# Optimization experiments

Measured on AMD Instinct MI355X. Metric: run time of the kernel, lower is better.

## Reference

```python
import jax, jax.numpy as jnp
import numpy as np

N_NODES = 40000
N_EDGES = 640000
D = 128
NEG_SLOPE = 0.2
EPS = 0.0  # init_eps=0, learn_eps=False -> constant buffer


def setup_inputs() -> dict:
    key = jax.random.key(0)
    ks = jax.random.split(key, 9)
    return {
        "feat": jax.random.normal(ks[0], (N_NODES, D), dtype=jnp.float32),
        "W_src": jax.random.normal(ks[1], (D, D), dtype=jnp.float32) * 0.1,
        "W_dst": jax.random.normal(ks[2], (D, D), dtype=jnp.float32) * 0.1,
        "W_src2": jax.random.normal(ks[3], (D, D), dtype=jnp.float32) * 0.1,
        "W_dst2": jax.random.normal(ks[4], (D, D), dtype=jnp.float32) * 0.1,
        "attn_l": jax.random.normal(ks[5], (D,), dtype=jnp.float32) * 0.1,
        "attn_r": jax.random.normal(ks[6], (D,), dtype=jnp.float32) * 0.1,
        "src": jax.random.randint(ks[7], (N_EDGES,), 0, N_NODES, dtype=jnp.int32),
        "dst": jax.random.randint(ks[8], (N_EDGES,), 0, N_NODES, dtype=jnp.int32),
    }


def reference(feat, W_src, W_dst, W_src2, W_dst2, attn_l, attn_r, src, dst):
    n = feat.shape[0]
    # Four linear projections (no bias), nn.Linear applies x @ W.T
    fs1 = feat @ W_src.T    # [N, D] -> messages for GIN sum
    fd1 = feat @ W_dst.T    # [N, D] -> self term
    fs2 = feat @ W_src2.T   # [N, D] -> attention-weighted messages
    fd2 = feat @ W_dst2.T   # [N, D]

    # GAT-style per-node attention logits
    el = jnp.sum(fs2 * attn_l, axis=-1)  # [N]
    er = jnp.sum(fd2 * attn_r, axis=-1)  # [N]

    # Per-edge score: u_add_v + leaky_relu
    e = el[src] + er[dst]                                   # [E]
    e = jnp.where(e >= 0, e, NEG_SLOPE * e)

    # edge_softmax: segment-wise softmax over edges grouped by dst
    seg_max = jax.ops.segment_max(e, dst, num_segments=n)   # [N]
    seg_max = jnp.where(jnp.isfinite(seg_max), seg_max, 0.0)
    ex = jnp.exp(e - seg_max[dst])                          # [E]
    denom = jax.ops.segment_sum(ex, dst, num_segments=n)    # [N]
    a = ex / denom[dst]                                     # [E]

    # update_all(copy_u, sum): plain neighbor sum of fs1
    neigh = jax.ops.segment_sum(fs1[src], dst, num_segments=n)            # [N, D]
    # update_all(u_mul_e, sum): attention-weighted sum of fs2
    add_ft = jax.ops.segment_sum(fs2[src] * a[:, None], dst, num_segments=n)  # [N, D]

    rst = (1.0 + EPS) * fd1 + neigh + add_ft
    return rst
```

## Files before the change

kernel.cpp:

```cpp
#include <hip/hip_runtime.h>
#include <math.h>

#define N_NODES 40000
#define N_EDGES 640000
#define D 128
#define NEG_SLOPE 0.2f
#define BCAP 64

typedef __bf16 bf16x8 __attribute__((ext_vector_type(8)));
typedef float f32x4 __attribute__((ext_vector_type(4)));

__device__ __forceinline__ unsigned short f2bf(float f) {
    unsigned int u = __float_as_uint(f);
    return (unsigned short)((u + 0x7fffu + ((u >> 16) & 1u)) >> 16);
}
__device__ __forceinline__ float bflo(unsigned int u) { return __uint_as_float(u << 16); }
__device__ __forceinline__ float bfhi(unsigned int u) { return __uint_as_float(u & 0xffff0000u); }

__global__ void k_zero(uint4* __restrict__ cnt4) {
    int i = blockIdx.x * 256 + threadIdx.x;
    if (i < 10000) cnt4[i] = make_uint4(0, 0, 0, 0);
}

__global__ void k_init_fill(const float* __restrict__ Ws, const float* __restrict__ Ws2,
                            const float* __restrict__ Wd, const float* __restrict__ Wd2,
                            const float* __restrict__ attn_l, const float* __restrict__ attn_r,
                            unsigned short* __restrict__ Wfrag,
                            float* __restrict__ v_l, float* __restrict__ v_r,
                            const int* __restrict__ src, const int* __restrict__ dst,
                            int* __restrict__ cnt, unsigned short* __restrict__ bucket,
                            const float* __restrict__ feat, unsigned int* __restrict__ featb) {
    if (blockIdx.x >= 2693) {
        int t = (blockIdx.x - 2693) * 256 + threadIdx.x;
        if (t < 640000) {
            const float* fp = feat + (size_t)t * 8;
            float4 p = *(const float4*)fp;
            float4 q = *(const float4*)(fp + 4);
            uint4 u;
            u.x = (unsigned int)f2bf(p.x) | ((unsigned int)f2bf(p.y) << 16);
            u.y = (unsigned int)f2bf(p.z) | ((unsigned int)f2bf(p.w) << 16);
            u.z = (unsigned int)f2bf(q.x) | ((unsigned int)f2bf(q.y) << 16);
            u.w = (unsigned int)f2bf(q.z) | ((unsigned int)f2bf(q.w) << 16);
            *(uint4*)(featb + (size_t)t * 4) = u;
        }
        return;
    }
    if (blockIdx.x >= 193) {
        int e = (blockIdx.x - 193) * 256 + threadIdx.x;
        if (e < N_EDGES) {
            int d = dst[e];
            int slot = atomicAdd(&cnt[d], 1);
            if (slot < BCAP) bucket[(size_t)d * BCAP + slot] = (unsigned short)src[e];
        }
        return;
    }
    if (blockIdx.x == 192) {
        int t = threadIdx.x;
        if (t < 128) {
            float s = 0.0f;
            for (int j = 0; j < D; ++j) s += attn_l[j] * Ws2[j * D + t];
            v_l[t] = s;
        } else {
            int k = t - 128;
            float s = 0.0f;
            for (int j = 0; j < D; ++j) s += attn_r[j] * Wd2[j * D + k];
            v_r[k] = s;
        }
        return;
    }
    int idx = blockIdx.x * 256 + threadIdx.x;
    int e    = idx & 7;
    int lane = (idx >> 3) & 63;
    int ks   = (idx >> 9) & 3;
    int ct   = (idx >> 11) & 7;
    int m    = idx >> 14;
    int col  = ct * 16 + (lane & 15);
    int k    = ks * 32 + (lane >> 4) * 8 + e;
    const float* W = (m == 0) ? Ws : (m == 1) ? Ws2 : Wd;
    Wfrag[idx] = f2bf(W[col * D + k]);
}

__global__ __launch_bounds__(256) void k_gemm_pre(
    const float* __restrict__ feat, const unsigned short* __restrict__ Wfrag,
    const float* __restrict__ vl, const float* __restrict__ vr,
    float* __restrict__ out, float* __restrict__ el, float* __restrict__ er)
{
    const int lane = threadIdx.x & 63;
    const int wave = threadIdx.x >> 6;
    const int row0 = blockIdx.x * 64 + wave * 16;
    const int arow = row0 + (lane & 15);
    const int kb   = (lane >> 4) * 8;

    bf16x8 a[4];
    float sl = 0.f, sr = 0.f;
    #pragma unroll
    for (int ks = 0; ks < 4; ++ks) {
        const float* fp = feat + (size_t)arow * D + ks * 32 + kb;
        float4 p = *(const float4*)fp;
        float4 q = *(const float4*)(fp + 4);
        bf16x8 av;
        av[0] = (__bf16)p.x; av[1] = (__bf16)p.y; av[2] = (__bf16)p.z; av[3] = (__bf16)p.w;
        av[4] = (__bf16)q.x; av[5] = (__bf16)q.y; av[6] = (__bf16)q.z; av[7] = (__bf16)q.w;
        a[ks] = av;
        const float* vlp = vl + ks * 32 + kb;
        const float* vrp = vr + ks * 32 + kb;
        float4 l0 = *(const float4*)vlp, l1 = *(const float4*)(vlp + 4);
        float4 r0 = *(const float4*)vrp, r1 = *(const float4*)(vrp + 4);
        sl += p.x*l0.x + p.y*l0.y + p.z*l0.z + p.w*l0.w
            + q.x*l1.x + q.y*l1.y + q.z*l1.z + q.w*l1.w;
        sr += p.x*r0.x + p.y*r0.y + p.z*r0.z + p.w*r0.w
            + q.x*r1.x + q.y*r1.y + q.z*r1.z + q.w*r1.w;
    }
    sl += __shfl_xor(sl, 16); sl += __shfl_xor(sl, 32);
    sr += __shfl_xor(sr, 16); sr += __shfl_xor(sr, 32);
    if (lane < 16) { el[row0 + lane] = sl; er[row0 + lane] = sr; }

    const bf16x8* wf = (const bf16x8*)Wfrag + (size_t)(2 * 8 * 4) * 64;
    f32x4 acc[8];
    #pragma unroll
    for (int ct = 0; ct < 8; ++ct) acc[ct] = (f32x4){0.f, 0.f, 0.f, 0.f};
    #pragma unroll
    for (int ks = 0; ks < 4; ++ks) {
        #pragma unroll
        for (int ct = 0; ct < 8; ++ct) {
            bf16x8 b = wf[(size_t)(ct * 4 + ks) * 64 + lane];
            acc[ct] = __builtin_amdgcn_mfma_f32_16x16x32_bf16(a[ks], b, acc[ct], 0, 0, 0);
        }
    }

    const int rbase = row0 + (lane >> 4) * 4;
    const int cbase = lane & 15;
    #pragma unroll
    for (int ct = 0; ct < 8; ++ct)
        #pragma unroll
        for (int r = 0; r < 4; ++r)
            out[(size_t)(rbase + r) * D + ct * 16 + cbase] = acc[ct][r];
}

__global__ __launch_bounds__(256) void k_aggregate(
    const int* __restrict__ cnt, const unsigned short* __restrict__ bucket,
    const float* __restrict__ el, const float* __restrict__ er,
    const unsigned int* __restrict__ featb,
    unsigned int* __restrict__ agg1b, unsigned int* __restrict__ agg2b)
{
    const int node = blockIdx.x * 4 + (threadIdx.x >> 6);
    const int lane = threadIdx.x & 63;
    if (node >= N_NODES) return;
    int deg = cnt[node];
    deg = (deg > BCAP) ? BCAP : deg;

    const int q = lane & 15;
    const int g = lane >> 4;
    float A1[8], A2[8];
    #pragma unroll
    for (int c = 0; c < 8; ++c) { A1[c] = 0.f; A2[c] = 0.f; }

    if (deg > 0) {
        const int base = node * BCAP;
        const float ern = er[node];
        int s_l = 0;
        float e = -INFINITY;
        if (lane < deg) {
            s_l = bucket[base + lane];
            e = el[s_l] + ern;
            e = (e >= 0.f) ? e : NEG_SLOPE * e;
        }
        float mx = e;
        #pragma unroll
        for (int w = 32; w >= 1; w >>= 1) mx = fmaxf(mx, __shfl_xor(mx, w));
        float p = (lane < deg) ? __expf(e - mx) : 0.f;
        float ssum = p;
        #pragma unroll
        for (int w = 32; w >= 1; w >>= 1) ssum += __shfl_xor(ssum, w);
        float a_l = p / ssum;

        const int dup = (deg + 15) & ~15;
        for (int i = 0; i < dup; i += 16) {
            uint4 v[4];
            float av[4], wf[4];
            #pragma unroll
            for (int j = 0; j < 4; ++j) {
                int eidx = i + j * 4 + g;
                int s = __shfl(s_l, eidx);
                av[j] = __shfl(a_l, eidx);
                wf[j] = (eidx < deg) ? 1.0f : 0.0f;
                v[j] = *(const uint4*)(featb + (size_t)s * 64 + q * 4);
            }
            #pragma unroll
            for (int j = 0; j < 4; ++j) {
                float x0 = bflo(v[j].x), x1 = bfhi(v[j].x);
                float x2 = bflo(v[j].y), x3 = bfhi(v[j].y);
                float x4 = bflo(v[j].z), x5 = bfhi(v[j].z);
                float x6 = bflo(v[j].w), x7 = bfhi(v[j].w);
                A1[0] += wf[j] * x0; A2[0] += av[j] * x0;
                A1[1] += wf[j] * x1; A2[1] += av[j] * x1;
                A1[2] += wf[j] * x2; A2[2] += av[j] * x2;
                A1[3] += wf[j] * x3; A2[3] += av[j] * x3;
                A1[4] += wf[j] * x4; A2[4] += av[j] * x4;
                A1[5] += wf[j] * x5; A2[5] += av[j] * x5;
                A1[6] += wf[j] * x6; A2[6] += av[j] * x6;
                A1[7] += wf[j] * x7; A2[7] += av[j] * x7;
            }
        }
        #pragma unroll
        for (int c = 0; c < 8; ++c) {
            A1[c] += __shfl_xor(A1[c], 16); A1[c] += __shfl_xor(A1[c], 32);
            A2[c] += __shfl_xor(A2[c], 16); A2[c] += __shfl_xor(A2[c], 32);
        }
    }

    if (lane < 16) {
        uint4 u1, u2;
        u1.x = (unsigned int)f2bf(A1[0]) | ((unsigned int)f2bf(A1[1]) << 16);
        u1.y = (unsigned int)f2bf(A1[2]) | ((unsigned int)f2bf(A1[3]) << 16);
        u1.z = (unsigned int)f2bf(A1[4]) | ((unsigned int)f2bf(A1[5]) << 16);
        u1.w = (unsigned int)f2bf(A1[6]) | ((unsigned int)f2bf(A1[7]) << 16);
        u2.x = (unsigned int)f2bf(A2[0]) | ((unsigned int)f2bf(A2[1]) << 16);
        u2.y = (unsigned int)f2bf(A2[2]) | ((unsigned int)f2bf(A2[3]) << 16);
        u2.z = (unsigned int)f2bf(A2[4]) | ((unsigned int)f2bf(A2[5]) << 16);
        u2.w = (unsigned int)f2bf(A2[6]) | ((unsigned int)f2bf(A2[7]) << 16);
        *(uint4*)(agg1b + (size_t)node * 64 + q * 4) = u1;
        *(uint4*)(agg2b + (size_t)node * 64 + q * 4) = u2;
    }
}

__global__ __launch_bounds__(256) void k_gemm_post(
    const unsigned int* __restrict__ agg1b, const unsigned int* __restrict__ agg2b,
    const unsigned short* __restrict__ Wfrag, float* __restrict__ out)
{
    const int lane = threadIdx.x & 63;
    const int wave = threadIdx.x >> 6;
    const int row0 = blockIdx.x * 64 + wave * 16;
    const int arow = row0 + (lane & 15);
    const int kb   = (lane >> 4) * 8;

    bf16x8 a1[4], a2[4];
    #pragma unroll
    for (int ks = 0; ks < 4; ++ks) {
        a1[ks] = *(const bf16x8*)((const unsigned short*)agg1b + (size_t)arow * D + ks * 32 + kb);
        a2[ks] = *(const bf16x8*)((const unsigned short*)agg2b + (size_t)arow * D + ks * 32 + kb);
    }

    const bf16x8* wf0 = (const bf16x8*)Wfrag;
    const bf16x8* wf1 = (const bf16x8*)Wfrag + (size_t)(8 * 4) * 64;
    f32x4 acc[8];
    #pragma unroll
    for (int ct = 0; ct < 8; ++ct) acc[ct] = (f32x4){0.f, 0.f, 0.f, 0.f};
    #pragma unroll
    for (int ks = 0; ks < 4; ++ks) {
        #pragma unroll
        for (int ct = 0; ct < 8; ++ct) {
            acc[ct] = __builtin_amdgcn_mfma_f32_16x16x32_bf16(a1[ks], wf0[(size_t)(ct * 4 + ks) * 64 + lane], acc[ct], 0, 0, 0);
            acc[ct] = __builtin_amdgcn_mfma_f32_16x16x32_bf16(a2[ks], wf1[(size_t)(ct * 4 + ks) * 64 + lane], acc[ct], 0, 0, 0);
        }
    }

    const int rbase = row0 + (lane >> 4) * 4;
    const int cbase = lane & 15;
    #pragma unroll
    for (int ct = 0; ct < 8; ++ct)
        #pragma unroll
        for (int r = 0; r < 4; ++r) {
            size_t o = (size_t)(rbase + r) * D + ct * 16 + cbase;
            out[o] += acc[ct][r];
        }
}

extern "C" void kernel_launch(void* const* d_in, const int* in_sizes, int n_in,
                              void* d_out, int out_size, void* d_ws, size_t ws_size,
                              hipStream_t stream) {
    const float* feat   = (const float*)d_in[0];
    const float* W_src  = (const float*)d_in[1];
    const float* W_dst  = (const float*)d_in[2];
    const float* W_src2 = (const float*)d_in[3];
    const float* W_dst2 = (const float*)d_in[4];
    const float* attn_l = (const float*)d_in[5];
    const float* attn_r = (const float*)d_in[6];
    const int*   src    = (const int*)d_in[7];
    const int*   dst    = (const int*)d_in[8];
    float* out = (float*)d_out;

    char* w = (char*)d_ws;
    float* v_l = (float*)w;                       w += 128 * 4;
    float* v_r = (float*)w;                       w += 128 * 4;
    float* el  = (float*)w;                       w += N_NODES * 4;
    float* er  = (float*)w;                       w += N_NODES * 4;
    int* cnt   = (int*)w;                         w += N_NODES * 4;
    unsigned int* featb = (unsigned int*)w;       w += (size_t)N_NODES * 64 * 4;
    unsigned int* agg1b = (unsigned int*)w;       w += (size_t)N_NODES * 64 * 4;
    unsigned int* agg2b = (unsigned int*)w;       w += (size_t)N_NODES * 64 * 4;
    unsigned short* bucket = (unsigned short*)w;  w += (size_t)N_NODES * BCAP * 2;
    unsigned short* Wfrag = (unsigned short*)w;   w += 3 * 8 * 4 * 64 * 8 * 2;

    k_zero<<<40, 256, 0, stream>>>((uint4*)cnt);

    k_init_fill<<<5193, 256, 0, stream>>>(
        W_src, W_src2, W_dst, W_dst2, attn_l, attn_r, Wfrag, v_l, v_r,
        src, dst, cnt, bucket, feat, featb);

    k_gemm_pre<<<625, 256, 0, stream>>>(feat, Wfrag, v_l, v_r, out, el, er);

    k_aggregate<<<(N_NODES + 3) / 4, 256, 0, stream>>>(cnt, bucket, el, er,
                                                       featb, agg1b, agg2b);

    k_gemm_post<<<625, 256, 0, stream>>>(agg1b, agg2b, Wfrag, out);
}
```

Baseline: 102.2 us.

## Fuse self-term GEMM into post-aggregation GEMM and compute logits during bf16 conversion

Result: faster. 96.21 us (-5.8%).

```diff
diff --git a/kernel.cpp b/kernel.cpp
--- a/kernel.cpp
+++ b/kernel.cpp
@@ -17,44 +17,11 @@
 __device__ __forceinline__ float bflo(unsigned int u) { return __uint_as_float(u << 16); }
 __device__ __forceinline__ float bfhi(unsigned int u) { return __uint_as_float(u & 0xffff0000u); }
 
-__global__ void k_zero(uint4* __restrict__ cnt4) {
-    int i = blockIdx.x * 256 + threadIdx.x;
-    if (i < 10000) cnt4[i] = make_uint4(0, 0, 0, 0);
-}
-
-__global__ void k_init_fill(const float* __restrict__ Ws, const float* __restrict__ Ws2,
-                            const float* __restrict__ Wd, const float* __restrict__ Wd2,
-                            const float* __restrict__ attn_l, const float* __restrict__ attn_r,
-                            unsigned short* __restrict__ Wfrag,
-                            float* __restrict__ v_l, float* __restrict__ v_r,
-                            const int* __restrict__ src, const int* __restrict__ dst,
-                            int* __restrict__ cnt, unsigned short* __restrict__ bucket,
-                            const float* __restrict__ feat, unsigned int* __restrict__ featb) {
-    if (blockIdx.x >= 2693) {
-        int t = (blockIdx.x - 2693) * 256 + threadIdx.x;
-        if (t < 640000) {
-            const float* fp = feat + (size_t)t * 8;
-            float4 p = *(const float4*)fp;
-            float4 q = *(const float4*)(fp + 4);
-            uint4 u;
-            u.x = (unsigned int)f2bf(p.x) | ((unsigned int)f2bf(p.y) << 16);
-            u.y = (unsigned int)f2bf(p.z) | ((unsigned int)f2bf(p.w) << 16);
-            u.z = (unsigned int)f2bf(q.x) | ((unsigned int)f2bf(q.y) << 16);
-            u.w = (unsigned int)f2bf(q.z) | ((unsigned int)f2bf(q.w) << 16);
-            *(uint4*)(featb + (size_t)t * 4) = u;
-        }
-        return;
-    }
-    if (blockIdx.x >= 193) {
-        int e = (blockIdx.x - 193) * 256 + threadIdx.x;
-        if (e < N_EDGES) {
-            int d = dst[e];
-            int slot = atomicAdd(&cnt[d], 1);
-            if (slot < BCAP) bucket[(size_t)d * BCAP + slot] = (unsigned short)src[e];
-        }
-        return;
-    }
-    if (blockIdx.x == 192) {
+__global__ void k_zero_v(uint4* __restrict__ cnt4,
+                         const float* __restrict__ Ws2, const float* __restrict__ Wd2,
+                         const float* __restrict__ attn_l, const float* __restrict__ attn_r,
+                         float* __restrict__ v_l, float* __restrict__ v_r) {
+    if (blockIdx.x == 40) {
         int t = threadIdx.x;
         if (t < 128) {
             float s = 0.0f;
@@ -68,6 +35,56 @@
         }
         return;
     }
+    int i = blockIdx.x * 256 + threadIdx.x;
+    if (i < 10000) cnt4[i] = make_uint4(0, 0, 0, 0);
+}
+
+__global__ void k_setup(const float* __restrict__ Ws, const float* __restrict__ Ws2,
+                        const float* __restrict__ Wd,
+                        unsigned short* __restrict__ Wfrag,
+                        const float* __restrict__ v_l, const float* __restrict__ v_r,
+                        const int* __restrict__ src, const int* __restrict__ dst,
+                        int* __restrict__ cnt, unsigned short* __restrict__ bucket,
+                        const float* __restrict__ feat, unsigned int* __restrict__ featb,
+                        float* __restrict__ el, float* __restrict__ er) {
+    if (blockIdx.x >= 2692) {
+        int idx = blockIdx.x - 2692;
+        int row = idx * 16 + (threadIdx.x >> 4);
+        int c   = threadIdx.x & 15;
+        const float* fp = feat + (size_t)row * D + c * 8;
+        float4 p = *(const float4*)fp;
+        float4 q = *(const float4*)(fp + 4);
+        uint4 u;
+        u.x = (unsigned int)f2bf(p.x) | ((unsigned int)f2bf(p.y) << 16);
+        u.y = (unsigned int)f2bf(p.z) | ((unsigned int)f2bf(p.w) << 16);
+        u.z = (unsigned int)f2bf(q.x) | ((unsigned int)f2bf(q.y) << 16);
+        u.w = (unsigned int)f2bf(q.z) | ((unsigned int)f2bf(q.w) << 16);
+        *(uint4*)(featb + (size_t)row * 64 + c * 4) = u;
+        const float* vlp = v_l + c * 8;
+        const float* vrp = v_r + c * 8;
+        float4 l0 = *(const float4*)vlp, l1 = *(const float4*)(vlp + 4);
+        float4 r0 = *(const float4*)vrp, r1 = *(const float4*)(vrp + 4);
+        float sl = p.x*l0.x + p.y*l0.y + p.z*l0.z + p.w*l0.w
+                 + q.x*l1.x + q.y*l1.y + q.z*l1.z + q.w*l1.w;
+        float sr = p.x*r0.x + p.y*r0.y + p.z*r0.z + p.w*r0.w
+                 + q.x*r1.x + q.y*r1.y + q.z*r1.z + q.w*r1.w;
+        #pragma unroll
+        for (int w = 1; w <= 8; w <<= 1) {
+            sl += __shfl_xor(sl, w);
+            sr += __shfl_xor(sr, w);
+        }
+        if (c == 0) { el[row] = sl; er[row] = sr; }
+        return;
+    }
+    if (blockIdx.x >= 192) {
+        int e = (blockIdx.x - 192) * 256 + threadIdx.x;
+        if (e < N_EDGES) {
+            int d = dst[e];
+            int slot = atomicAdd(&cnt[d], 1);
+            if (slot < BCAP) bucket[(size_t)d * BCAP + slot] = (unsigned short)src[e];
+        }
+        return;
+    }
     int idx = blockIdx.x * 256 + threadIdx.x;
     int e    = idx & 7;
     int lane = (idx >> 3) & 63;
@@ -78,63 +95,6 @@
     int k    = ks * 32 + (lane >> 4) * 8 + e;
     const float* W = (m == 0) ? Ws : (m == 1) ? Ws2 : Wd;
     Wfrag[idx] = f2bf(W[col * D + k]);
-}
-
-__global__ __launch_bounds__(256) void k_gemm_pre(
-    const float* __restrict__ feat, const unsigned short* __restrict__ Wfrag,
-    const float* __restrict__ vl, const float* __restrict__ vr,
-    float* __restrict__ out, float* __restrict__ el, float* __restrict__ er)
-{
-    const int lane = threadIdx.x & 63;
-    const int wave = threadIdx.x >> 6;
-    const int row0 = blockIdx.x * 64 + wave * 16;
-    const int arow = row0 + (lane & 15);
-    const int kb   = (lane >> 4) * 8;
-
-    bf16x8 a[4];
-    float sl = 0.f, sr = 0.f;
-    #pragma unroll
-    for (int ks = 0; ks < 4; ++ks) {
-        const float* fp = feat + (size_t)arow * D + ks * 32 + kb;
-        float4 p = *(const float4*)fp;
-        float4 q = *(const float4*)(fp + 4);
-        bf16x8 av;
-        av[0] = (__bf16)p.x; av[1] = (__bf16)p.y; av[2] = (__bf16)p.z; av[3] = (__bf16)p.w;
-        av[4] = (__bf16)q.x; av[5] = (__bf16)q.y; av[6] = (__bf16)q.z; av[7] = (__bf16)q.w;
-        a[ks] = av;
-        const float* vlp = vl + ks * 32 + kb;
-        const float* vrp = vr + ks * 32 + kb;
-        float4 l0 = *(const float4*)vlp, l1 = *(const float4*)(vlp + 4);
-        float4 r0 = *(const float4*)vrp, r1 = *(const float4*)(vrp + 4);
-        sl += p.x*l0.x + p.y*l0.y + p.z*l0.z + p.w*l0.w
-            + q.x*l1.x + q.y*l1.y + q.z*l1.z + q.w*l1.w;
-        sr += p.x*r0.x + p.y*r0.y + p.z*r0.z + p.w*r0.w
-            + q.x*r1.x + q.y*r1.y + q.z*r1.z + q.w*r1.w;
-    }
-    sl += __shfl_xor(sl, 16); sl += __shfl_xor(sl, 32);
-    sr += __shfl_xor(sr, 16); sr += __shfl_xor(sr, 32);
-    if (lane < 16) { el[row0 + lane] = sl; er[row0 + lane] = sr; }
-
-    const bf16x8* wf = (const bf16x8*)Wfrag + (size_t)(2 * 8 * 4) * 64;
-    f32x4 acc[8];
-    #pragma unroll
-    for (int ct = 0; ct < 8; ++ct) acc[ct] = (f32x4){0.f, 0.f, 0.f, 0.f};
-    #pragma unroll
-    for (int ks = 0; ks < 4; ++ks) {
-        #pragma unroll
-        for (int ct = 0; ct < 8; ++ct) {
-            bf16x8 b = wf[(size_t)(ct * 4 + ks) * 64 + lane];
-            acc[ct] = __builtin_amdgcn_mfma_f32_16x16x32_bf16(a[ks], b, acc[ct], 0, 0, 0);
-        }
-    }
-
-    const int rbase = row0 + (lane >> 4) * 4;
-    const int cbase = lane & 15;
-    #pragma unroll
-    for (int ct = 0; ct < 8; ++ct)
-        #pragma unroll
-        for (int r = 0; r < 4; ++r)
-            out[(size_t)(rbase + r) * D + ct * 16 + cbase] = acc[ct][r];
 }
 
 __global__ __launch_bounds__(256) void k_aggregate(
@@ -224,46 +184,53 @@
     }
 }
 
-__global__ __launch_bounds__(256) void k_gemm_post(
+__global__ __launch_bounds__(256) void k_gemm_all(
+    const unsigned int* __restrict__ featb,
     const unsigned int* __restrict__ agg1b, const unsigned int* __restrict__ agg2b,
     const unsigned short* __restrict__ Wfrag, float* __restrict__ out)
 {
     const int lane = threadIdx.x & 63;
     const int wave = threadIdx.x >> 6;
-    const int row0 = blockIdx.x * 64 + wave * 16;
+    const int tile = blockIdx.x >> 1;
+    const int cth  = (blockIdx.x & 1) * 4;
+    const int row0 = tile * 64 + wave * 16;
     const int arow = row0 + (lane & 15);
-    const int kb   = (lane >> 4) * 8;
-
-    bf16x8 a1[4], a2[4];
+    const int koff = (lane >> 4) * 4;
+
+    bf16x8 af[4], a1[4], a2[4];
     #pragma unroll
     for (int ks = 0; ks < 4; ++ks) {
-        a1[ks] = *(const bf16x8*)((const unsigned short*)agg1b + (size_t)arow * D + ks * 32 + kb);
-        a2[ks] = *(const bf16x8*)((const unsigned short*)agg2b + (size_t)arow * D + ks * 32 + kb);
+        size_t o = (size_t)arow * 64 + ks * 16 + koff;
+        af[ks] = *(const bf16x8*)(featb + o);
+        a1[ks] = *(const bf16x8*)(agg1b + o);
+        a2[ks] = *(const bf16x8*)(agg2b + o);
     }
 
     const bf16x8* wf0 = (const bf16x8*)Wfrag;
-    const bf16x8* wf1 = (const bf16x8*)Wfrag + (size_t)(8 * 4) * 64;
-    f32x4 acc[8];
-    #pragma unroll
-    for (int ct = 0; ct < 8; ++ct) acc[ct] = (f32x4){0.f, 0.f, 0.f, 0.f};
+    const bf16x8* wf1 = wf0 + (size_t)(8 * 4) * 64;
+    const bf16x8* wf2 = wf0 + (size_t)(2 * 8 * 4) * 64;
+
+    f32x4 acc[4];
+    #pragma unroll
+    for (int c = 0; c < 4; ++c) acc[c] = (f32x4){0.f, 0.f, 0.f, 0.f};
     #pragma unroll
     for (int ks = 0; ks < 4; ++ks) {
         #pragma unroll
-        for (int ct = 0; ct < 8; ++ct) {
-            acc[ct] = __builtin_amdgcn_mfma_f32_16x16x32_bf16(a1[ks], wf0[(size_t)(ct * 4 + ks) * 64 + lane], acc[ct], 0, 0, 0);
-            acc[ct] = __builtin_amdgcn_mfma_f32_16x16x32_bf16(a2[ks], wf1[(size_t)(ct * 4 + ks) * 64 + lane], acc[ct], 0, 0, 0);
+        for (int c = 0; c < 4; ++c) {
+            const size_t bo = (size_t)((cth + c) * 4 + ks) * 64 + lane;
+            acc[c] = __builtin_amdgcn_mfma_f32_16x16x32_bf16(af[ks], wf2[bo], acc[c], 0, 0, 0);
+            acc[c] = __builtin_amdgcn_mfma_f32_16x16x32_bf16(a1[ks], wf0[bo], acc[c], 0, 0, 0);
+            acc[c] = __builtin_amdgcn_mfma_f32_16x16x32_bf16(a2[ks], wf1[bo], acc[c], 0, 0, 0);
         }
     }
 
     const int rbase = row0 + (lane >> 4) * 4;
     const int cbase = lane & 15;
     #pragma unroll
-    for (int ct = 0; ct < 8; ++ct)
-        #pragma unroll
-        for (int r = 0; r < 4; ++r) {
-            size_t o = (size_t)(rbase + r) * D + ct * 16 + cbase;
-            out[o] += acc[ct][r];
-        }
+    for (int c = 0; c < 4; ++c)
+        #pragma unroll
+        for (int r = 0; r < 4; ++r)
+            out[(size_t)(rbase + r) * D + (cth + c) * 16 + cbase] = acc[c][r];
 }
 
 extern "C" void kernel_launch(void* const* d_in, const int* in_sizes, int n_in,
@@ -292,16 +259,13 @@
     unsigned short* bucket = (unsigned short*)w;  w += (size_t)N_NODES * BCAP * 2;
     unsigned short* Wfrag = (unsigned short*)w;   w += 3 * 8 * 4 * 64 * 8 * 2;
 
-    k_zero<<<40, 256, 0, stream>>>((uint4*)cnt);
-
-    k_init_fill<<<5193, 256, 0, stream>>>(
-        W_src, W_src2, W_dst, W_dst2, attn_l, attn_r, Wfrag, v_l, v_r,
-        src, dst, cnt, bucket, feat, featb);
-
-    k_gemm_pre<<<625, 256, 0, stream>>>(feat, Wfrag, v_l, v_r, out, el, er);
+    k_zero_v<<<41, 256, 0, stream>>>((uint4*)cnt, W_src2, W_dst2, attn_l, attn_r, v_l, v_r);
+
+    k_setup<<<5192, 256, 0, stream>>>(W_src, W_src2, W_dst, Wfrag, v_l, v_r,
+                                      src, dst, cnt, bucket, feat, featb, el, er);
 
     k_aggregate<<<(N_NODES + 3) / 4, 256, 0, stream>>>(cnt, bucket, el, er,
                                                        featb, agg1b, agg2b);
 
-    k_gemm_post<<<625, 256, 0, stream>>>(agg1b, agg2b, Wfrag, out);
-}
+    k_gemm_all<<<1250, 256, 0, stream>>>(featb, agg1b, agg2b, Wfrag, out);
+}
```
